# Performance work log

Hardware: AMD Instinct MI355X
Metric: run time of the kernel (lower is better)

Reference implementation:

```python
import jax, jax.numpy as jnp
import numpy as np

N_P = 8192
N_T = 8192
# layer widths from GPNPolicyNet.__init__: (8,8)->(8,8)->(16,16)->(64,64)->(16,16)
DIMS = [(8, 8, 8, 8), (8, 8, 16, 16), (16, 16, 64, 64), (64, 64, 16, 16)]


def setup_inputs() -> dict:
    key = jax.random.key(0)
    ks = iter(jax.random.split(key, 64))
    inp = {
        "p": jax.random.normal(next(ks), (N_P, 8), jnp.float32),
        "t": jax.random.normal(next(ks), (N_T, 8), jnp.float32),
        # sparse-ish 0/1 Petri incidence stored dense (as in the torch module)
        "adj": (jax.random.uniform(next(ks), (N_P, N_T)) < 0.005).astype(jnp.float32),
    }
    for i, (lp_in, lt_in, lp_out, lt_out) in enumerate(DIMS, start=1):
        c = lp_in + lt_in
        sc = 1.0 / np.sqrt(c)
        inp[f"w_p{i}"] = jax.random.uniform(next(ks), (c, lp_out), jnp.float32, -sc, sc)
        inp[f"b_p{i}"] = jnp.zeros((lp_out,), jnp.float32)
        inp[f"w_t{i}"] = jax.random.uniform(next(ks), (c, lt_out), jnp.float32, -sc, sc)
        inp[f"b_t{i}"] = jnp.zeros((lt_out,), jnp.float32)
    sc = 1.0 / np.sqrt(32.0)
    inp["w_ac"] = jax.random.uniform(next(ks), (32, 1), jnp.float32, -sc, sc)
    inp["b_ac"] = jnp.zeros((1,), jnp.float32)
    return inp


def _gcpn(p, t, adj, wp, bp, wt, bt):
    agg_t = adj @ t        # [n_p, lt_in]: places gather from incident transitions
    agg_p = adj.T @ p      # [n_t, lp_in]: transitions gather from incident places
    p_out = jax.nn.relu(jnp.concatenate([p, agg_t], axis=-1) @ wp + bp)
    t_out = jax.nn.relu(jnp.concatenate([agg_p, t], axis=-1) @ wt + bt)
    return p_out, t_out


def reference(p, t, adj,
              w_p1, b_p1, w_t1, b_t1,
              w_p2, b_p2, w_t2, b_t2,
              w_p3, b_p3, w_t3, b_t3,
              w_p4, b_p4, w_t4, b_t4,
              w_ac, b_ac):
    p, t = _gcpn(p, t, adj, w_p1, b_p1, w_t1, b_t1)
    p, t = _gcpn(p, t, adj, w_p2, b_p2, w_t2, b_t2)
    p, t = _gcpn(p, t, adj, w_p3, b_p3, w_t3, b_t3)
    p, t = _gcpn(p, t, adj, w_p4, b_p4, w_t4, b_t4)
    x = jnp.concatenate([adj.T @ p, t], axis=-1)  # [n_t, 32]
    logits = (x @ w_ac + b_ac)[:, 0]              # [n_t]
    return jax.nn.softmax(logits, axis=-1)        # firing distribution over transitions
```

## Files before the change

### kernel.cpp

```cpp
#include <hip/hip_runtime.h>
#include <math.h>

#define N_NODES 8192
#define CAP 128
#define NBLK 2048
#define NWAVE (NBLK * 4)
#define NGRP 32
#define GSZ (NBLK / NGRP)

__device__ __forceinline__ void asf(float* p, float v) {
    __hip_atomic_store(p, v, __ATOMIC_RELAXED, __HIP_MEMORY_SCOPE_AGENT);
}
__device__ __forceinline__ unsigned uadd(unsigned* p, unsigned v) {
    return __hip_atomic_fetch_add(p, v, __ATOMIC_RELAXED, __HIP_MEMORY_SCOPE_AGENT);
}
__device__ __forceinline__ unsigned uld(const unsigned* p) {
    return __hip_atomic_load(p, __ATOMIC_RELAXED, __HIP_MEMORY_SCOPE_AGENT);
}
__device__ __forceinline__ void ust(unsigned* p, unsigned v) {
    __hip_atomic_store(p, v, __ATOMIC_RELAXED, __HIP_MEMORY_SCOPE_AGENT);
}
__device__ __forceinline__ int get_xcd() {
    int x;
    asm volatile("s_getreg_b32 %0, hwreg(HW_REG_XCC_ID)" : "=s"(x));
    return x & 7;
}

struct Params {
    const float4* adj4;
    const float* p; const float* t;
    const float* w_p1; const float* b_p1; const float* w_t1; const float* b_t1;
    const float* w_p2; const float* b_p2; const float* w_t2; const float* b_t2;
    const float* w_p3; const float* b_p3; const float* w_t3; const float* b_t3;
    const float* w_p4; const float* b_p4; const float* w_t4; const float* b_t4;
    const float* w_ac; const float* b_ac;
    int* rowCnt; int* rowIdx; int* colCnt; int* colIdx;
    float* pA; float* pB; float* tA; float* tB; float* logits;
    unsigned* c1;
    unsigned* c2;
    unsigned* epoch;
    unsigned* claim;
    unsigned* done;
    float4* out4;
};

__device__ __forceinline__ void gbar(const Params& P, int ph) {
    __syncthreads();
    if (threadIdx.x == 0) {
        unsigned o = uadd(P.c1 + (ph * NGRP + (blockIdx.x & (NGRP - 1))) * 16, 1u);
        if (o == (GSZ - 1)) {
            unsigned o2 = uadd(P.c2 + ph * 16, 1u);
            if (o2 == NGRP - 1) ust(P.epoch, (unsigned)(ph + 1));
        }
        while (uld(P.epoch) < (unsigned)(ph + 1))
            __builtin_amdgcn_s_sleep(2);
        const int xcd = get_xcd();
        unsigned* cl = P.claim + (ph * 8 + xcd) * 16;
        unsigned* dn = P.done  + (ph * 8 + xcd) * 16;
        if (uadd(cl, 1u) == 0) {
            asm volatile("buffer_inv sc0 sc1" ::: "memory");
            asm volatile("s_waitcnt vmcnt(0)" ::: "memory");
            ust(dn, 1u);
        } else {
            asm volatile("buffer_inv sc0" ::: "memory");
            asm volatile("s_waitcnt vmcnt(0)" ::: "memory");
            while (uld(dn) == 0)
                __builtin_amdgcn_s_sleep(2);
        }
    }
    __syncthreads();
}
__device__ __forceinline__ void gbar_last(const Params& P, int ph) {
    __syncthreads();
    if (threadIdx.x == 0) {
        unsigned o = uadd(P.c1 + (ph * NGRP + (blockIdx.x & (NGRP - 1))) * 16, 1u);
        if (o == (GSZ - 1)) {
            unsigned o2 = uadd(P.c2 + ph * 16, 1u);
            if (o2 == NGRP - 1) ust(P.epoch, (unsigned)(ph + 1));
        }
        if (blockIdx.x == 0) {
            while (uld(P.epoch) < (unsigned)(ph + 1))
                __builtin_amdgcn_s_sleep(2);
            asm volatile("buffer_inv sc0 sc1" ::: "memory");
            asm volatile("s_waitcnt vmcnt(0)" ::: "memory");
        }
    }
    __syncthreads();
}

__global__ __launch_bounds__(256) void phaseA_k(Params P) {
    const int gid = blockIdx.x * 256 + threadIdx.x;
#pragma unroll 1
    for (int k = 0; k < 32; k += 4) {
        float4 w[4];
#pragma unroll
        for (int u = 0; u < 4; ++u)
            w[u] = P.adj4[(size_t)(k + u) * (NBLK * 256) + gid];
#pragma unroll
        for (int u = 0; u < 4; ++u) {
            const int fi = (k + u) * (NBLK * 256) + gid;
            const int r  = fi >> 11;
            const int c4 = fi & 2047;
            if (w[u].x != 0.f || w[u].y != 0.f || w[u].z != 0.f || w[u].w != 0.f) {
                float vals[4] = {w[u].x, w[u].y, w[u].z, w[u].w};
#pragma unroll
                for (int e = 0; e < 4; ++e) {
                    if (vals[e] != 0.f) {
                        int c = c4 * 4 + e;
                        int pr = atomicAdd(&P.rowCnt[r], 1);
                        if (pr < CAP) P.rowIdx[r * CAP + pr] = c;
                        int pc = atomicAdd(&P.colCnt[c], 1);
                        if (pc < CAP) P.colIdx[c * CAP + pc] = r;
                    }
                }
            }
        }
    }
}

template <int CI, int CO, bool RELU, bool TONLY>
__device__ __forceinline__ void layer_step(
    const Params& P,
    const float* __restrict__ pIn, const float* __restrict__ tIn,
    const float* __restrict__ Wp, const float* __restrict__ Bp,
    const float* __restrict__ Wt, const float* __restrict__ Bt,
    float* __restrict__ pOut, float* __restrict__ tOut,
    float* sWp, float* sWt, float* sBp, float* sBt, float (*sIn)[128])
{
    constexpr int C = 2 * CI;
    constexpr int G = 64 / CI;
    for (int k = threadIdx.x; k < C * CO; k += 256) { sWp[k] = Wp[k]; sWt[k] = Wt[k]; }
    if (threadIdx.x < CO) { sBp[threadIdx.x] = Bp[threadIdx.x]; sBt[threadIdx.x] = Bt[threadIdx.x]; }
    __syncthreads();

    const int rl = threadIdx.x >> 6, lane = threadIdx.x & 63;
    const int wg = blockIdx.x * 4 + rl;
    const int feat = lane & (CI - 1);
    const int grp = lane / CI;
    constexpr int NT = TONLY ? N_NODES : 2 * N_NODES;

#pragma unroll 1
    for (int task = wg; task < NT; task += NWAVE) {
        const bool tSide = TONLY ? true : (task >= N_NODES);
        const int row = TONLY ? task : (tSide ? task - N_NODES : task);
        const float* self_in = tSide ? tIn : pIn;
        const float* oth_in  = tSide ? pIn : tIn;
        const int* cnt  = tSide ? P.colCnt : P.rowCnt;
        const int* idxl = tSide ? P.colIdx : P.rowIdx;
        const float* sW  = tSide ? sWt : sWp;
        const float* sBv = tSide ? sBt : sBp;

        int m = cnt[row];
        if (m > CAP) m = CAP;
        const int* __restrict__ lst = idxl + row * CAP;

        const int len = (m + G - 1) / G;
        const int s0 = grp * len;
        const int s1 = min(s0 + len, m);
        float acc = 0.f;
        int s = s0;
        for (; s + 8 <= s1; s += 8) {
            int j0 = lst[s],     j1 = lst[s + 1], j2 = lst[s + 2], j3 = lst[s + 3];
            int j4 = lst[s + 4], j5 = lst[s + 5], j6 = lst[s + 6], j7 = lst[s + 7];
            float a0 = oth_in[j0 * CI + feat];
            float a1 = oth_in[j1 * CI + feat];
            float a2 = oth_in[j2 * CI + feat];
            float a3 = oth_in[j3 * CI + feat];
            float a4 = oth_in[j4 * CI + feat];
            float a5 = oth_in[j5 * CI + feat];
            float a6 = oth_in[j6 * CI + feat];
            float a7 = oth_in[j7 * CI + feat];
            acc += ((a0 + a1) + (a2 + a3)) + ((a4 + a5) + (a6 + a7));
        }
        for (; s + 4 <= s1; s += 4) {
            int j0 = lst[s], j1 = lst[s + 1], j2 = lst[s + 2], j3 = lst[s + 3];
            float a0 = oth_in[j0 * CI + feat];
            float a1 = oth_in[j1 * CI + feat];
            float a2 = oth_in[j2 * CI + feat];
            float a3 = oth_in[j3 * CI + feat];
            acc += (a0 + a1) + (a2 + a3);
        }
        for (; s < s1; ++s) acc += oth_in[lst[s] * CI + feat];
#pragma unroll
        for (int off = 32; off >= CI; off >>= 1) acc += __shfl_down(acc, off);

        if (lane < CI) {
            const int aggOff  = tSide ? 0 : CI;
            const int selfOff = tSide ? CI : 0;
            sIn[rl][aggOff + lane]  = acc;
            sIn[rl][selfOff + lane] = self_in[row * CI + lane];
        }
        __syncthreads();
        if (lane < CO) {
            float o = sBv[lane];
#pragma unroll
            for (int k = 0; k < C; ++k) o += sIn[rl][k] * sW[k * CO + lane];
            if (RELU) o = fmaxf(o, 0.f);
            asf(&(tSide ? tOut : pOut)[row * CO + lane], o);
        }
        __syncthreads();
    }
}

__device__ __forceinline__ void softmax_dev(const Params& P, float* red) {
    const int tid = threadIdx.x;
    float va[32];
    float mx = -INFINITY;
#pragma unroll
    for (int k = 0; k < 32; ++k) {
        va[k] = P.logits[tid * 32 + k];
        mx = fmaxf(mx, va[k]);
    }
    red[tid] = mx;
    __syncthreads();
    for (int s2 = 128; s2 > 0; s2 >>= 1) {
        if (tid < s2) red[tid] = fmaxf(red[tid], red[tid + s2]);
        __syncthreads();
    }
    mx = red[0];
    __syncthreads();
    float sum = 0.f;
#pragma unroll
    for (int k = 0; k < 32; ++k) {
        va[k] = __expf(va[k] - mx);
        sum += va[k];
    }
    red[tid] = sum;
    __syncthreads();
    for (int s2 = 128; s2 > 0; s2 >>= 1) {
        if (tid < s2) red[tid] += red[tid + s2];
        __syncthreads();
    }
    float inv = 1.f / red[0];
    float4* o4 = P.out4 + tid * 8;
#pragma unroll
    for (int k = 0; k < 8; ++k) {
        o4[k] = make_float4(va[4 * k] * inv, va[4 * k + 1] * inv,
                            va[4 * k + 2] * inv, va[4 * k + 3] * inv);
    }
}

__global__ __launch_bounds__(256, 8) void gcn_layers(Params P) {
    __shared__ float sW[2][2048];
    __shared__ float sB[2][64];
    __shared__ float sIn[4][128];
    __shared__ float red[256];

    layer_step<8, 8, true, false>(P, P.p, P.t, P.w_p1, P.b_p1, P.w_t1, P.b_t1,
                                  P.pA, P.tA, sW[0], sW[1], sB[0], sB[1], sIn);
    gbar(P, 0);
    layer_step<8, 16, true, false>(P, P.pA, P.tA, P.w_p2, P.b_p2, P.w_t2, P.b_t2,
                                   P.pB, P.tB, sW[0], sW[1], sB[0], sB[1], sIn);
    gbar(P, 1);
    layer_step<16, 64, true, false>(P, P.pB, P.tB, P.w_p3, P.b_p3, P.w_t3, P.b_t3,
                                    P.pA, P.tA, sW[0], sW[1], sB[0], sB[1], sIn);
    gbar(P, 2);
    layer_step<64, 16, true, false>(P, P.pA, P.tA, P.w_p4, P.b_p4, P.w_t4, P.b_t4,
                                    P.pB, P.tB, sW[0], sW[1], sB[0], sB[1], sIn);
    gbar(P, 3);
    layer_step<16, 1, false, true>(P, P.pB, P.tB, P.w_ac, P.b_ac, P.w_ac, P.b_ac,
                                   P.logits, P.logits, sW[0], sW[1], sB[0], sB[1], sIn);
    gbar_last(P, 4);
    if (blockIdx.x == 0) softmax_dev(P, red);
}

template <int CI, int CO, bool RELU, bool TONLY>
__global__ __launch_bounds__(256) void layer_k(Params P,
    const float* pIn, const float* tIn,
    const float* Wp, const float* Bp, const float* Wt, const float* Bt,
    float* pOut, float* tOut)
{
    __shared__ float sW[2][2048];
    __shared__ float sB[2][64];
    __shared__ float sIn[4][128];
    layer_step<CI, CO, RELU, TONLY>(P, pIn, tIn, Wp, Bp, Wt, Bt, pOut, tOut,
                                    sW[0], sW[1], sB[0], sB[1], sIn);
}
__global__ __launch_bounds__(256) void softmax_k(Params P) {
    __shared__ float red[256];
    softmax_dev(P, red);
}

extern "C" void kernel_launch(void* const* d_in, const int* in_sizes, int n_in,
                              void* d_out, int out_size, void* d_ws, size_t ws_size,
                              hipStream_t stream) {
    char* ws = (char*)d_ws;
    Params prm;
    prm.adj4 = (const float4*)d_in[2];
    prm.p    = (const float*)d_in[0];
    prm.t    = (const float*)d_in[1];
    prm.w_p1 = (const float*)d_in[3];  prm.b_p1 = (const float*)d_in[4];
    prm.w_t1 = (const float*)d_in[5];  prm.b_t1 = (const float*)d_in[6];
    prm.w_p2 = (const float*)d_in[7];  prm.b_p2 = (const float*)d_in[8];
    prm.w_t2 = (const float*)d_in[9];  prm.b_t2 = (const float*)d_in[10];
    prm.w_p3 = (const float*)d_in[11]; prm.b_p3 = (const float*)d_in[12];
    prm.w_t3 = (const float*)d_in[13]; prm.b_t3 = (const float*)d_in[14];
    prm.w_p4 = (const float*)d_in[15]; prm.b_p4 = (const float*)d_in[16];
    prm.w_t4 = (const float*)d_in[17]; prm.b_t4 = (const float*)d_in[18];
    prm.w_ac = (const float*)d_in[19]; prm.b_ac = (const float*)d_in[20];

    const size_t MB = 1024 * 1024;
    prm.rowCnt = (int*)(ws);
    prm.colCnt = (int*)(ws + 32768);
    prm.c1     = (unsigned*)(ws + 65536);
    prm.c2     = (unsigned*)(ws + 81920);
    prm.epoch  = (unsigned*)(ws + 86016);
    prm.claim  = (unsigned*)(ws + 90112);
    prm.done   = (unsigned*)(ws + 94208);
    prm.rowIdx = (int*)(ws + 1 * MB);
    prm.colIdx = (int*)(ws + 5 * MB);
    prm.pA     = (float*)(ws + 9 * MB);
    prm.pB     = (float*)(ws + 11 * MB);
    prm.tA     = (float*)(ws + 13 * MB);
    prm.tB     = (float*)(ws + 15 * MB);
    prm.logits = (float*)(ws + 17 * MB);
    prm.out4   = (float4*)d_out;

    hipMemsetAsync(ws, 0, 98304, stream);

    phaseA_k<<<NBLK, 256, 0, stream>>>(prm);

    void* args[] = { (void*)&prm };
    hipError_t e = hipLaunchCooperativeKernel(reinterpret_cast<void*>(&gcn_layers),
                                              dim3(NBLK), dim3(256), args, 0, stream);
    if (e != hipSuccess) {
        layer_k<8, 8, true, false><<<NBLK, 256, 0, stream>>>(
            prm, prm.p, prm.t, prm.w_p1, prm.b_p1, prm.w_t1, prm.b_t1, prm.pA, prm.tA);
        layer_k<8, 16, true, false><<<NBLK, 256, 0, stream>>>(
            prm, prm.pA, prm.tA, prm.w_p2, prm.b_p2, prm.w_t2, prm.b_t2, prm.pB, prm.tB);
        layer_k<16, 64, true, false><<<NBLK, 256, 0, stream>>>(
            prm, prm.pB, prm.tB, prm.w_p3, prm.b_p3, prm.w_t3, prm.b_t3, prm.pA, prm.tA);
        layer_k<64, 16, true, false><<<NBLK, 256, 0, stream>>>(
            prm, prm.pA, prm.tA, prm.w_p4, prm.b_p4, prm.w_t4, prm.b_t4, prm.pB, prm.tB);
        layer_k<16, 1, false, true><<<NBLK, 256, 0, stream>>>(
            prm, prm.pB, prm.tB, prm.w_ac, prm.b_ac, prm.w_ac, prm.b_ac, prm.logits, prm.logits);
        softmax_k<<<1, 256, 0, stream>>>(prm);
    }
}
```

Measured before the change: 560.2 us.

## Replace cooperative persistent kernel with per-layer launches and wider softmax

Drops the cooperative persistent kernel and its hand-rolled grid barriers with cache invalidations. Each GCN layer now runs as its own launch, one wave per node and a grid sized to the node count, with shared memory sized per layer from template constants. Softmax moves to a single 1024-thread block reading float4. Barrier spinning and cache invalidation go away, and the smaller shared footprint may raise occupancy, at the cost of five extra kernel launches and losing data reuse across layers inside one kernel.

```diff
diff --git a/kernel.cpp b/kernel.cpp
--- a/kernel.cpp
+++ b/kernel.cpp
@@ -3,28 +3,7 @@
 
 #define N_NODES 8192
 #define CAP 128
-#define NBLK 2048
-#define NWAVE (NBLK * 4)
-#define NGRP 32
-#define GSZ (NBLK / NGRP)
-
-__device__ __forceinline__ void asf(float* p, float v) {
-    __hip_atomic_store(p, v, __ATOMIC_RELAXED, __HIP_MEMORY_SCOPE_AGENT);
-}
-__device__ __forceinline__ unsigned uadd(unsigned* p, unsigned v) {
-    return __hip_atomic_fetch_add(p, v, __ATOMIC_RELAXED, __HIP_MEMORY_SCOPE_AGENT);
-}
-__device__ __forceinline__ unsigned uld(const unsigned* p) {
-    return __hip_atomic_load(p, __ATOMIC_RELAXED, __HIP_MEMORY_SCOPE_AGENT);
-}
-__device__ __forceinline__ void ust(unsigned* p, unsigned v) {
-    __hip_atomic_store(p, v, __ATOMIC_RELAXED, __HIP_MEMORY_SCOPE_AGENT);
-}
-__device__ __forceinline__ int get_xcd() {
-    int x;
-    asm volatile("s_getreg_b32 %0, hwreg(HW_REG_XCC_ID)" : "=s"(x));
-    return x & 7;
-}
+#define ABLK 2048
 
 struct Params {
     const float4* adj4;
@@ -36,57 +15,8 @@
     const float* w_ac; const float* b_ac;
     int* rowCnt; int* rowIdx; int* colCnt; int* colIdx;
     float* pA; float* pB; float* tA; float* tB; float* logits;
-    unsigned* c1;
-    unsigned* c2;
-    unsigned* epoch;
-    unsigned* claim;
-    unsigned* done;
     float4* out4;
 };
-
-__device__ __forceinline__ void gbar(const Params& P, int ph) {
-    __syncthreads();
-    if (threadIdx.x == 0) {
-        unsigned o = uadd(P.c1 + (ph * NGRP + (blockIdx.x & (NGRP - 1))) * 16, 1u);
-        if (o == (GSZ - 1)) {
-            unsigned o2 = uadd(P.c2 + ph * 16, 1u);
-            if (o2 == NGRP - 1) ust(P.epoch, (unsigned)(ph + 1));
-        }
-        while (uld(P.epoch) < (unsigned)(ph + 1))
-            __builtin_amdgcn_s_sleep(2);
-        const int xcd = get_xcd();
-        unsigned* cl = P.claim + (ph * 8 + xcd) * 16;
-        unsigned* dn = P.done  + (ph * 8 + xcd) * 16;
-        if (uadd(cl, 1u) == 0) {
-            asm volatile("buffer_inv sc0 sc1" ::: "memory");
-            asm volatile("s_waitcnt vmcnt(0)" ::: "memory");
-            ust(dn, 1u);
-        } else {
-            asm volatile("buffer_inv sc0" ::: "memory");
-            asm volatile("s_waitcnt vmcnt(0)" ::: "memory");
-            while (uld(dn) == 0)
-                __builtin_amdgcn_s_sleep(2);
-        }
-    }
-    __syncthreads();
-}
-__device__ __forceinline__ void gbar_last(const Params& P, int ph) {
-    __syncthreads();
-    if (threadIdx.x == 0) {
-        unsigned o = uadd(P.c1 + (ph * NGRP + (blockIdx.x & (NGRP - 1))) * 16, 1u);
-        if (o == (GSZ - 1)) {
-            unsigned o2 = uadd(P.c2 + ph * 16, 1u);
-            if (o2 == NGRP - 1) ust(P.epoch, (unsigned)(ph + 1));
-        }
-        if (blockIdx.x == 0) {
-            while (uld(P.epoch) < (unsigned)(ph + 1))
-                __builtin_amdgcn_s_sleep(2);
-            asm volatile("buffer_inv sc0 sc1" ::: "memory");
-            asm volatile("s_waitcnt vmcnt(0)" ::: "memory");
-        }
-    }
-    __syncthreads();
-}
 
 __global__ __launch_bounds__(256) void phaseA_k(Params P) {
     const int gid = blockIdx.x * 256 + threadIdx.x;
@@ -95,10 +25,10 @@
         float4 w[4];
 #pragma unroll
         for (int u = 0; u < 4; ++u)
-            w[u] = P.adj4[(size_t)(k + u) * (NBLK * 256) + gid];
+            w[u] = P.adj4[(size_t)(k + u) * (ABLK * 256) + gid];
 #pragma unroll
         for (int u = 0; u < 4; ++u) {
-            const int fi = (k + u) * (NBLK * 256) + gid;
+            const int fi = (k + u) * (ABLK * 256) + gid;
             const int r  = fi >> 11;
             const int c4 = fi & 2047;
             if (w[u].x != 0.f || w[u].y != 0.f || w[u].z != 0.f || w[u].w != 0.f) {
@@ -119,166 +49,119 @@
 }
 
 template <int CI, int CO, bool RELU, bool TONLY>
-__device__ __forceinline__ void layer_step(
-    const Params& P,
+__global__ __launch_bounds__(256) void layer_k(Params P,
     const float* __restrict__ pIn, const float* __restrict__ tIn,
     const float* __restrict__ Wp, const float* __restrict__ Bp,
     const float* __restrict__ Wt, const float* __restrict__ Bt,
-    float* __restrict__ pOut, float* __restrict__ tOut,
-    float* sWp, float* sWt, float* sBp, float* sBt, float (*sIn)[128])
+    float* __restrict__ pOut, float* __restrict__ tOut)
 {
     constexpr int C = 2 * CI;
     constexpr int G = 64 / CI;
+    __shared__ float sWp[C * CO];
+    __shared__ float sWt[C * CO];
+    __shared__ float sBp[CO];
+    __shared__ float sBt[CO];
+    __shared__ float sIn[4][C];
+
     for (int k = threadIdx.x; k < C * CO; k += 256) { sWp[k] = Wp[k]; sWt[k] = Wt[k]; }
     if (threadIdx.x < CO) { sBp[threadIdx.x] = Bp[threadIdx.x]; sBt[threadIdx.x] = Bt[threadIdx.x]; }
     __syncthreads();
 
     const int rl = threadIdx.x >> 6, lane = threadIdx.x & 63;
-    const int wg = blockIdx.x * 4 + rl;
+    const int task = blockIdx.x * 4 + rl;
     const int feat = lane & (CI - 1);
-    const int grp = lane / CI;
-    constexpr int NT = TONLY ? N_NODES : 2 * N_NODES;
-
-#pragma unroll 1
-    for (int task = wg; task < NT; task += NWAVE) {
-        const bool tSide = TONLY ? true : (task >= N_NODES);
-        const int row = TONLY ? task : (tSide ? task - N_NODES : task);
-        const float* self_in = tSide ? tIn : pIn;
-        const float* oth_in  = tSide ? pIn : tIn;
-        const int* cnt  = tSide ? P.colCnt : P.rowCnt;
-        const int* idxl = tSide ? P.colIdx : P.rowIdx;
-        const float* sW  = tSide ? sWt : sWp;
-        const float* sBv = tSide ? sBt : sBp;
-
-        int m = cnt[row];
-        if (m > CAP) m = CAP;
-        const int* __restrict__ lst = idxl + row * CAP;
-
-        const int len = (m + G - 1) / G;
-        const int s0 = grp * len;
-        const int s1 = min(s0 + len, m);
-        float acc = 0.f;
-        int s = s0;
-        for (; s + 8 <= s1; s += 8) {
-            int j0 = lst[s],     j1 = lst[s + 1], j2 = lst[s + 2], j3 = lst[s + 3];
-            int j4 = lst[s + 4], j5 = lst[s + 5], j6 = lst[s + 6], j7 = lst[s + 7];
-            float a0 = oth_in[j0 * CI + feat];
-            float a1 = oth_in[j1 * CI + feat];
-            float a2 = oth_in[j2 * CI + feat];
-            float a3 = oth_in[j3 * CI + feat];
-            float a4 = oth_in[j4 * CI + feat];
-            float a5 = oth_in[j5 * CI + feat];
-            float a6 = oth_in[j6 * CI + feat];
-            float a7 = oth_in[j7 * CI + feat];
-            acc += ((a0 + a1) + (a2 + a3)) + ((a4 + a5) + (a6 + a7));
-        }
-        for (; s + 4 <= s1; s += 4) {
-            int j0 = lst[s], j1 = lst[s + 1], j2 = lst[s + 2], j3 = lst[s + 3];
-            float a0 = oth_in[j0 * CI + feat];
-            float a1 = oth_in[j1 * CI + feat];
-            float a2 = oth_in[j2 * CI + feat];
-            float a3 = oth_in[j3 * CI + feat];
-            acc += (a0 + a1) + (a2 + a3);
-        }
-        for (; s < s1; ++s) acc += oth_in[lst[s] * CI + feat];
-#pragma unroll
-        for (int off = 32; off >= CI; off >>= 1) acc += __shfl_down(acc, off);
-
-        if (lane < CI) {
-            const int aggOff  = tSide ? 0 : CI;
-            const int selfOff = tSide ? CI : 0;
-            sIn[rl][aggOff + lane]  = acc;
-            sIn[rl][selfOff + lane] = self_in[row * CI + lane];
-        }
+    const int grp  = lane / CI;
+
+    const bool tSide = TONLY ? true : (task >= N_NODES);
+    const int row = TONLY ? task : (tSide ? task - N_NODES : task);
+    const float* self_in = tSide ? tIn : pIn;
+    const float* oth_in  = tSide ? pIn : tIn;
+    const int* cnt  = tSide ? P.colCnt : P.rowCnt;
+    const int* idxl = tSide ? P.colIdx : P.rowIdx;
+    const float* sW  = tSide ? sWt : sWp;
+    const float* sBv = tSide ? sBt : sBp;
+
+    int m = cnt[row];
+    if (m > CAP) m = CAP;
+    const int* __restrict__ lst = idxl + row * CAP;
+
+    const int len = (m + G - 1) / G;
+    const int s0 = grp * len;
+    const int s1 = min(s0 + len, m);
+    float acc = 0.f;
+    int s = s0;
+    for (; s + 8 <= s1; s += 8) {
+        int j0 = lst[s],     j1 = lst[s + 1], j2 = lst[s + 2], j3 = lst[s + 3];
+        int j4 = lst[s + 4], j5 = lst[s + 5], j6 = lst[s + 6], j7 = lst[s + 7];
+        float a0 = oth_in[j0 * CI + feat];
+        float a1 = oth_in[j1 * CI + feat];
+        float a2 = oth_in[j2 * CI + feat];
+        float a3 = oth_in[j3 * CI + feat];
+        float a4 = oth_in[j4 * CI + feat];
+        float a5 = oth_in[j5 * CI + feat];
+        float a6 = oth_in[j6 * CI + feat];
+        float a7 = oth_in[j7 * CI + feat];
+        acc += ((a0 + a1) + (a2 + a3)) + ((a4 + a5) + (a6 + a7));
+    }
+    for (; s + 4 <= s1; s += 4) {
+        int j0 = lst[s], j1 = lst[s + 1], j2 = lst[s + 2], j3 = lst[s + 3];
+        float a0 = oth_in[j0 * CI + feat];
+        float a1 = oth_in[j1 * CI + feat];
+        float a2 = oth_in[j2 * CI + feat];
+        float a3 = oth_in[j3 * CI + feat];
+        acc += (a0 + a1) + (a2 + a3);
+    }
+    for (; s < s1; ++s) acc += oth_in[lst[s] * CI + feat];
+#pragma unroll
+    for (int off = 32; off >= CI; off >>= 1) acc += __shfl_down(acc, off);
+
+    if (lane < CI) {
+        const int aggOff  = tSide ? 0 : CI;
+        const int selfOff = tSide ? CI : 0;
+        sIn[rl][aggOff + lane]  = acc;
+        sIn[rl][selfOff + lane] = self_in[row * CI + lane];
+    }
+    __syncthreads();
+    if (lane < CO) {
+        float o = sBv[lane];
+#pragma unroll
+        for (int k = 0; k < C; ++k) o += sIn[rl][k] * sW[k * CO + lane];
+        if (RELU) o = fmaxf(o, 0.f);
+        (tSide ? tOut : pOut)[row * CO + lane] = o;
+    }
+}
+
+__global__ __launch_bounds__(1024) void softmax_k(const float4* __restrict__ logits4,
+                                                  float4* __restrict__ out4) {
+    __shared__ float red[1024];
+    float4 a = logits4[threadIdx.x];
+    float4 b = logits4[threadIdx.x + 1024];
+    float mx = fmaxf(fmaxf(fmaxf(a.x, a.y), fmaxf(a.z, a.w)),
+                     fmaxf(fmaxf(b.x, b.y), fmaxf(b.z, b.w)));
+    red[threadIdx.x] = mx;
+    __syncthreads();
+    for (int s = 512; s > 0; s >>= 1) {
+        if (threadIdx.x < s) red[threadIdx.x] = fmaxf(red[threadIdx.x], red[threadIdx.x + s]);
         __syncthreads();
-        if (lane < CO) {
-            float o = sBv[lane];
-#pragma unroll
-            for (int k = 0; k < C; ++k) o += sIn[rl][k] * sW[k * CO + lane];
-            if (RELU) o = fmaxf(o, 0.f);
-            asf(&(tSide ? tOut : pOut)[row * CO + lane], o);
-        }
+    }
+    mx = red[0];
+    __syncthreads();
+    a.x = __expf(a.x - mx); a.y = __expf(a.y - mx);
+    a.z = __expf(a.z - mx); a.w = __expf(a.w - mx);
+    b.x = __expf(b.x - mx); b.y = __expf(b.y - mx);
+    b.z = __expf(b.z - mx); b.w = __expf(b.w - mx);
+    float sum = ((a.x + a.y) + (a.z + a.w)) + ((b.x + b.y) + (b.z + b.w));
+    red[threadIdx.x] = sum;
+    __syncthreads();
+    for (int s = 512; s > 0; s >>= 1) {
+        if (threadIdx.x < s) red[threadIdx.x] += red[threadIdx.x + s];
         __syncthreads();
     }
-}
-
-__device__ __forceinline__ void softmax_dev(const Params& P, float* red) {
-    const int tid = threadIdx.x;
-    float va[32];
-    float mx = -INFINITY;
-#pragma unroll
-    for (int k = 0; k < 32; ++k) {
-        va[k] = P.logits[tid * 32 + k];
-        mx = fmaxf(mx, va[k]);
-    }
-    red[tid] = mx;
-    __syncthreads();
-    for (int s2 = 128; s2 > 0; s2 >>= 1) {
-        if (tid < s2) red[tid] = fmaxf(red[tid], red[tid + s2]);
-        __syncthreads();
-    }
-    mx = red[0];
-    __syncthreads();
-    float sum = 0.f;
-#pragma unroll
-    for (int k = 0; k < 32; ++k) {
-        va[k] = __expf(va[k] - mx);
-        sum += va[k];
-    }
-    red[tid] = sum;
-    __syncthreads();
-    for (int s2 = 128; s2 > 0; s2 >>= 1) {
-        if (tid < s2) red[tid] += red[tid + s2];
-        __syncthreads();
-    }
     float inv = 1.f / red[0];
-    float4* o4 = P.out4 + tid * 8;
-#pragma unroll
-    for (int k = 0; k < 8; ++k) {
-        o4[k] = make_float4(va[4 * k] * inv, va[4 * k + 1] * inv,
-                            va[4 * k + 2] * inv, va[4 * k + 3] * inv);
-    }
-}
-
-__global__ __launch_bounds__(256, 8) void gcn_layers(Params P) {
-    __shared__ float sW[2][2048];
-    __shared__ float sB[2][64];
-    __shared__ float sIn[4][128];
-    __shared__ float red[256];
-
-    layer_step<8, 8, true, false>(P, P.p, P.t, P.w_p1, P.b_p1, P.w_t1, P.b_t1,
-                                  P.pA, P.tA, sW[0], sW[1], sB[0], sB[1], sIn);
-    gbar(P, 0);
-    layer_step<8, 16, true, false>(P, P.pA, P.tA, P.w_p2, P.b_p2, P.w_t2, P.b_t2,
-                                   P.pB, P.tB, sW[0], sW[1], sB[0], sB[1], sIn);
-    gbar(P, 1);
-    layer_step<16, 64, true, false>(P, P.pB, P.tB, P.w_p3, P.b_p3, P.w_t3, P.b_t3,
-                                    P.pA, P.tA, sW[0], sW[1], sB[0], sB[1], sIn);
-    gbar(P, 2);
-    layer_step<64, 16, true, false>(P, P.pA, P.tA, P.w_p4, P.b_p4, P.w_t4, P.b_t4,
-                                    P.pB, P.tB, sW[0], sW[1], sB[0], sB[1], sIn);
-    gbar(P, 3);
-    layer_step<16, 1, false, true>(P, P.pB, P.tB, P.w_ac, P.b_ac, P.w_ac, P.b_ac,
-                                   P.logits, P.logits, sW[0], sW[1], sB[0], sB[1], sIn);
-    gbar_last(P, 4);
-    if (blockIdx.x == 0) softmax_dev(P, red);
-}
-
-template <int CI, int CO, bool RELU, bool TONLY>
-__global__ __launch_bounds__(256) void layer_k(Params P,
-    const float* pIn, const float* tIn,
-    const float* Wp, const float* Bp, const float* Wt, const float* Bt,
-    float* pOut, float* tOut)
-{
-    __shared__ float sW[2][2048];
-    __shared__ float sB[2][64];
-    __shared__ float sIn[4][128];
-    layer_step<CI, CO, RELU, TONLY>(P, pIn, tIn, Wp, Bp, Wt, Bt, pOut, tOut,
-                                    sW[0], sW[1], sB[0], sB[1], sIn);
-}
-__global__ __launch_bounds__(256) void softmax_k(Params P) {
-    __shared__ float red[256];
-    softmax_dev(P, red);
+    a.x *= inv; a.y *= inv; a.z *= inv; a.w *= inv;
+    b.x *= inv; b.y *= inv; b.z *= inv; b.w *= inv;
+    out4[threadIdx.x] = a;
+    out4[threadIdx.x + 1024] = b;
 }
 
 extern "C" void kernel_launch(void* const* d_in, const int* in_sizes, int n_in,
@@ -302,11 +185,6 @@
     const size_t MB = 1024 * 1024;
     prm.rowCnt = (int*)(ws);
     prm.colCnt = (int*)(ws + 32768);
-    prm.c1     = (unsigned*)(ws + 65536);
-    prm.c2     = (unsigned*)(ws + 81920);
-    prm.epoch  = (unsigned*)(ws + 86016);
-    prm.claim  = (unsigned*)(ws + 90112);
-    prm.done   = (unsigned*)(ws + 94208);
     prm.rowIdx = (int*)(ws + 1 * MB);
     prm.colIdx = (int*)(ws + 5 * MB);
     prm.pA     = (float*)(ws + 9 * MB);
@@ -316,24 +194,20 @@
     prm.logits = (float*)(ws + 17 * MB);
     prm.out4   = (float4*)d_out;
 
-    hipMemsetAsync(ws, 0, 98304, stream);
-
-    phaseA_k<<<NBLK, 256, 0, stream>>>(prm);
-
-    void* args[] = { (void*)&prm };
-    hipError_t e = hipLaunchCooperativeKernel(reinterpret_cast<void*>(&gcn_layers),
-                                              dim3(NBLK), dim3(256), args, 0, stream);
-    if (e != hipSuccess) {
-        layer_k<8, 8, true, false><<<NBLK, 256, 0, stream>>>(
-            prm, prm.p, prm.t, prm.w_p1, prm.b_p1, prm.w_t1, prm.b_t1, prm.pA, prm.tA);
-        layer_k<8, 16, true, false><<<NBLK, 256, 0, stream>>>(
-            prm, prm.pA, prm.tA, prm.w_p2, prm.b_p2, prm.w_t2, prm.b_t2, prm.pB, prm.tB);
-        layer_k<16, 64, true, false><<<NBLK, 256, 0, stream>>>(
-            prm, prm.pB, prm.tB, prm.w_p3, prm.b_p3, prm.w_t3, prm.b_t3, prm.pA, prm.tA);
-        layer_k<64, 16, true, false><<<NBLK, 256, 0, stream>>>(
-            prm, prm.pA, prm.tA, prm.w_p4, prm.b_p4, prm.w_t4, prm.b_t4, prm.pB, prm.tB);
-        layer_k<16, 1, false, true><<<NBLK, 256, 0, stream>>>(
-            prm, prm.pB, prm.tB, prm.w_ac, prm.b_ac, prm.w_ac, prm.b_ac, prm.logits, prm.logits);
-        softmax_k<<<1, 256, 0, stream>>>(prm);
-    }
-}
+    hipMemsetAsync(ws, 0, 65536, stream);
+
+    phaseA_k<<<ABLK, 256, 0, stream>>>(prm);
+
+    layer_k<8, 8, true, false><<<N_NODES / 2, 256, 0, stream>>>(
+        prm, prm.p, prm.t, prm.w_p1, prm.b_p1, prm.w_t1, prm.b_t1, prm.pA, prm.tA);
+    layer_k<8, 16, true, false><<<N_NODES / 2, 256, 0, stream>>>(
+        prm, prm.pA, prm.tA, prm.w_p2, prm.b_p2, prm.w_t2, prm.b_t2, prm.pB, prm.tB);
+    layer_k<16, 64, true, false><<<N_NODES / 2, 256, 0, stream>>>(
+        prm, prm.pB, prm.tB, prm.w_p3, prm.b_p3, prm.w_t3, prm.b_t3, prm.pA, prm.tA);
+    layer_k<64, 16, true, false><<<N_NODES / 2, 256, 0, stream>>>(
+        prm, prm.pA, prm.tA, prm.w_p4, prm.b_p4, prm.w_t4, prm.b_t4, prm.pB, prm.tB);
+    layer_k<16, 1, false, true><<<N_NODES / 4, 256, 0, stream>>>(
+        prm, prm.pB, prm.tB, prm.w_ac, prm.b_ac, prm.w_ac, prm.b_ac, prm.logits, prm.logits);
+
+    softmax_k<<<1, 1024, 0, stream>>>((const float4*)prm.logits, prm.out4);
+}
```

Result: faster. 493.6 us (-11.9%).
